# Kernel tuning notes

Hardware: AMD Instinct MI355X
Metric: run time of the kernel (lower is better)

## Reference

```python
import jax, jax.numpy as jnp
import numpy as np

N = 524288          # number of residues
N_RESTYPE = 21      # 20 amino acids + UNK
MAX_RIGID = 8       # rigid groups per residue (backbone + 7 torsion frames)
MAX_ATOM = 24       # max atoms per residue


def setup_inputs() -> dict:
    key = jax.random.key(0)
    ks = jax.random.split(key, 6)
    residue_type = jax.random.randint(ks[0], (N,), 0, N_RESTYPE)
    bb = jax.random.normal(ks[1], (N, 4, 3), jnp.float32)
    pos0 = jax.random.normal(ks[2], (N, 3), jnp.float32)
    sc = jax.random.normal(ks[3], (N, MAX_RIGID - 1, 2), jnp.float32)
    # learned/constant per-residue-type tables (RIGID_* in the original)
    transforms_tensor = jax.random.normal(ks[4], (N_RESTYPE, MAX_RIGID, 4, 3), jnp.float32) * 0.5
    rigids_tensor = jax.random.normal(ks[5], (N_RESTYPE, MAX_ATOM, 3), jnp.float32)
    rng = np.random.default_rng(0)
    td = np.zeros((N_RESTYPE, MAX_RIGID), dtype=np.int32)
    for i in range(1, MAX_RIGID):  # parent frame index must precede the group
        td[:, i] = rng.integers(0, i, size=N_RESTYPE)
    transforms_dep = jnp.asarray(td)
    rigids_dep = jnp.asarray(rng.integers(0, MAX_RIGID, size=(N_RESTYPE, MAX_ATOM)),
                             dtype=jnp.int32)
    return {
        "residue_type": residue_type, "bb": bb, "pos0": pos0, "sc": sc,
        "transforms_tensor": transforms_tensor, "rigids_tensor": rigids_tensor,
        "transforms_dep": transforms_dep, "rigids_dep": rigids_dep,
    }


def combine_operations(X, Y):
    # X, Y: [..., 4, 3] rigid operators (rows 0:3 rotation, row 3 translation)
    R = X[..., :3, :] @ Y[..., :3, :]
    t = jnp.einsum('...ij,...j->...i', X[..., :3, :], Y[..., 3, :]) + X[..., 3, :]
    return jnp.concatenate([R, t[..., None, :]], axis=-2)


def reference(residue_type, bb, pos0, sc,
              transforms_tensor, rigids_tensor, transforms_dep, rigids_dep):
    transforms = transforms_tensor[residue_type]   # [N, MAX_RIGID, 4, 3]
    t_dep = transforms_dep[residue_type]           # [N, MAX_RIGID]
    rigids = rigids_tensor[residue_type]           # [N, MAX_ATOM, 3]
    r_dep = rigids_dep[residue_type]               # [N, MAX_ATOM]
    n = bb.shape[0]

    # group 0: backbone frame; translation offset by pos0
    opr0 = jnp.concatenate([bb[:, :3], (bb[:, 3] + pos0)[:, None, :]], axis=1)  # [N,4,3]
    # groups 1..: x-axis rotation from (cos, sin) torsion pairs, zero translation
    c, s = sc[..., 0], sc[..., 1]
    z = jnp.zeros_like(c)
    o = jnp.ones_like(c)
    rot_x = jnp.stack([
        jnp.stack([o, z, z], -1),
        jnp.stack([z, c, -s], -1),
        jnp.stack([z, s, c], -1),
        jnp.stack([z, z, z], -1),
    ], axis=-2)                                    # [N, MAX_RIGID-1, 4, 3]
    opr = jnp.concatenate([opr0[:, None], rot_x], axis=1)  # [N, MAX_RIGID, 4, 3]

    # compose with per-group fixed transforms
    opr = combine_operations(transforms, opr)

    # sequential dependency-chain gather-compose over rigid groups (small fixed loop)
    idx = jnp.arange(n)
    for i_tor in range(1, MAX_RIGID):
        prev = opr[idx, t_dep[:, i_tor]]                 # [N, 4, 3]
        opr = opr.at[:, i_tor].set(combine_operations(prev, opr[:, i_tor]))

    # per-atom frame gather and coordinate placement
    opr_atom = opr[idx[:, None], r_dep]                  # [N, MAX_ATOM, 4, 3]
    R = jnp.einsum('naij,naj->nai', opr_atom[:, :, :3], rigids) + opr_atom[:, :, 3]
    return R, opr[:, 0]
```

## Files before the change

### kernel.cpp

```cpp
#include <hip/hip_runtime.h>

#define NRT 21
#define NRIG 8
#define NATOM 24
#define BLK 256

struct Op { float r[3][3]; float t[3]; };

__device__ __forceinline__ void combine(const Op& X, const Op& Y, Op& D) {
#pragma unroll
    for (int i = 0; i < 3; ++i) {
#pragma unroll
        for (int j = 0; j < 3; ++j)
            D.r[i][j] = X.r[i][0]*Y.r[0][j] + X.r[i][1]*Y.r[1][j] + X.r[i][2]*Y.r[2][j];
        D.t[i] = X.r[i][0]*Y.t[0] + X.r[i][1]*Y.t[1] + X.r[i][2]*Y.t[2] + X.t[i];
    }
}

__device__ __forceinline__ void mixop(const Op& a, const Op& b, bool c, Op& o) {
#pragma unroll
    for (int i = 0; i < 3; ++i) {
#pragma unroll
        for (int j = 0; j < 3; ++j) o.r[i][j] = c ? b.r[i][j] : a.r[i][j];
        o.t[i] = c ? b.t[i] : a.t[i];
    }
}

__device__ __forceinline__ void select8(const Op opr[NRIG], int d, Op& out) {
    out = opr[0];
#pragma unroll
    for (int k = 1; k < NRIG; ++k) mixop(out, opr[k], d == k, out);
}

__global__ __launch_bounds__(BLK) void backbone_kernel(
    const int*   __restrict__ rtyp,
    const float* __restrict__ bb,
    const float* __restrict__ pos0,
    const float* __restrict__ sc,
    const float* __restrict__ tf_g,
    const float* __restrict__ rg_g,
    const int*   __restrict__ td_g,
    const int*   __restrict__ rd_g,
    float* __restrict__ out,
    int N)
{
    __shared__ float s_tf[96 * NRT];
    __shared__ float s_rg[72 * NRT];
    __shared__ int   s_td[NRIG * NRT];
    __shared__ int   s_rd[NATOM * NRT];

    for (int i = threadIdx.x; i < 96 * NRT; i += BLK) {
        int rt = i / 96, k = i - rt * 96;
        s_tf[k * NRT + rt] = tf_g[i];
    }
    for (int i = threadIdx.x; i < 72 * NRT; i += BLK) {
        int rt = i / 72, k = i - rt * 72;
        s_rg[k * NRT + rt] = rg_g[i];
    }
    for (int i = threadIdx.x; i < NRIG * NRT; i += BLK) {
        int rt = i / NRIG, k = i - rt * NRIG;
        s_td[k * NRT + rt] = td_g[i];
    }
    for (int i = threadIdx.x; i < NATOM * NRT; i += BLK) {
        int rt = i / NATOM, k = i - rt * NATOM;
        s_rd[k * NRT + rt] = rd_g[i];
    }
    __syncthreads();

    int n = blockIdx.x * BLK + threadIdx.x;
    if (n >= N) return;
    int rt = rtyp[n];

    const float4* bb4 = (const float4*)(bb + (size_t)n * 12);
    float4 b0 = bb4[0], b1 = bb4[1], b2 = bb4[2];
    const float* pp = pos0 + (size_t)n * 3;
    float p0 = pp[0], p1 = pp[1], p2 = pp[2];

    const float2* sc2 = (const float2*)(sc + (size_t)n * 14);
    float2 cs[7];
#pragma unroll
    for (int i = 0; i < 7; ++i) cs[i] = sc2[i];

    Op opr[NRIG];

    {
        Op X;
#pragma unroll
        for (int r = 0; r < 3; ++r)
#pragma unroll
            for (int c = 0; c < 3; ++c)
                X.r[r][c] = s_tf[(r * 3 + c) * NRT + rt];
#pragma unroll
        for (int c = 0; c < 3; ++c) X.t[c] = s_tf[(9 + c) * NRT + rt];
        Op Y;
        Y.r[0][0] = b0.x; Y.r[0][1] = b0.y; Y.r[0][2] = b0.z;
        Y.r[1][0] = b0.w; Y.r[1][1] = b1.x; Y.r[1][2] = b1.y;
        Y.r[2][0] = b1.z; Y.r[2][1] = b1.w; Y.r[2][2] = b2.x;
        Y.t[0] = b2.y + p0; Y.t[1] = b2.z + p1; Y.t[2] = b2.w + p2;
        combine(X, Y, opr[0]);
    }

#pragma unroll
    for (int i = 1; i < NRIG; ++i) {
        Op X;
#pragma unroll
        for (int r = 0; r < 3; ++r)
#pragma unroll
            for (int c = 0; c < 3; ++c)
                X.r[r][c] = s_tf[(i * 12 + r * 3 + c) * NRT + rt];
#pragma unroll
        for (int c = 0; c < 3; ++c) X.t[c] = s_tf[(i * 12 + 9 + c) * NRT + rt];
        float cv = cs[i - 1].x;
        float sv = cs[i - 1].y;
#pragma unroll
        for (int r = 0; r < 3; ++r) {
            opr[i].r[r][0] = X.r[r][0];
            opr[i].r[r][1] = X.r[r][1] * cv + X.r[r][2] * sv;
            opr[i].r[r][2] = X.r[r][2] * cv - X.r[r][1] * sv;
            opr[i].t[r]    = X.t[r];
        }
    }

#pragma unroll
    for (int i = 1; i < NRIG; ++i) {
        int d = s_td[i * NRT + rt];
        Op prev = opr[0];
#pragma unroll
        for (int k = 1; k < NRIG; ++k) {
            if (k < i) mixop(prev, opr[k], d == k, prev);
        }
        Op res;
        combine(prev, opr[i], res);
        opr[i] = res;
    }

    float* outR = out + (size_t)n * 72;
#pragma unroll
    for (int ch = 0; ch < 6; ++ch) {
        float w[12];
#pragma unroll
        for (int q = 0; q < 4; ++q) {
            int a = ch * 4 + q;
            int d = s_rd[a * NRT + rt];
            Op T;
            select8(opr, d, T);
            float vx = s_rg[(a * 3 + 0) * NRT + rt];
            float vy = s_rg[(a * 3 + 1) * NRT + rt];
            float vz = s_rg[(a * 3 + 2) * NRT + rt];
            w[q * 3 + 0] = T.r[0][0] * vx + T.r[0][1] * vy + T.r[0][2] * vz + T.t[0];
            w[q * 3 + 1] = T.r[1][0] * vx + T.r[1][1] * vy + T.r[1][2] * vz + T.t[1];
            w[q * 3 + 2] = T.r[2][0] * vx + T.r[2][1] * vy + T.r[2][2] * vz + T.t[2];
        }
        float4* dst = (float4*)(outR + ch * 12);
        dst[0] = make_float4(w[0], w[1], w[2],  w[3]);
        dst[1] = make_float4(w[4], w[5], w[6],  w[7]);
        dst[2] = make_float4(w[8], w[9], w[10], w[11]);
    }

    {
        float4* df = (float4*)(out + (size_t)N * 72 + (size_t)n * 12);
        df[0] = make_float4(opr[0].r[0][0], opr[0].r[0][1], opr[0].r[0][2], opr[0].r[1][0]);
        df[1] = make_float4(opr[0].r[1][1], opr[0].r[1][2], opr[0].r[2][0], opr[0].r[2][1]);
        df[2] = make_float4(opr[0].r[2][2], opr[0].t[0],    opr[0].t[1],    opr[0].t[2]);
    }
}

extern "C" void kernel_launch(void* const* d_in, const int* in_sizes, int n_in,
                              void* d_out, int out_size, void* d_ws, size_t ws_size,
                              hipStream_t stream) {
    const int*   rtyp = (const int*)d_in[0];
    const float* bb   = (const float*)d_in[1];
    const float* pos0 = (const float*)d_in[2];
    const float* sc   = (const float*)d_in[3];
    const float* tf   = (const float*)d_in[4];
    const float* rg   = (const float*)d_in[5];
    const int*   td   = (const int*)d_in[6];
    const int*   rd   = (const int*)d_in[7];
    int N = in_sizes[0];
    int grid = (N + BLK - 1) / BLK;
    backbone_kernel<<<grid, BLK, 0, stream>>>(rtyp, bb, pos0, sc, tf, rg, td, rd,
                                              (float*)d_out, N);
}
```

Measured before the change: 300.6 us.

## Gather per-atom frames from fp16-packed shared memory instead of register selects

After the dependency chain, each thread writes its eight composed frames into shared memory, packed as half2 pairs. Each atom then loads the frame it needs by index, replacing the 8-way register select chain that ran for every atom. The dependency tables shrink to u8, and the launch bounds now ask for two blocks. The per-thread shared buffer is large, which caps occupancy. Rounding frames and translations to fp16 loses precision and may break the output tolerance.

```diff
diff --git a/kernel.cpp b/kernel.cpp
--- a/kernel.cpp
+++ b/kernel.cpp
@@ -1,10 +1,14 @@
 #include <hip/hip_runtime.h>
+#include <hip/hip_fp16.h>
 
 #define NRT 21
 #define NRIG 8
 #define NATOM 24
 #define BLK 256
 
+typedef unsigned int u32;
+typedef unsigned char u8;
+
 struct Op { float r[3][3]; float t[3]; };
 
 __device__ __forceinline__ void combine(const Op& X, const Op& Y, Op& D) {
@@ -26,13 +30,18 @@
     }
 }
 
-__device__ __forceinline__ void select8(const Op opr[NRIG], int d, Op& out) {
-    out = opr[0];
-#pragma unroll
-    for (int k = 1; k < NRIG; ++k) mixop(out, opr[k], d == k, out);
-}
-
-__global__ __launch_bounds__(BLK) void backbone_kernel(
+__device__ __forceinline__ u32 pk(float a, float b) {
+    __half2 h = __floats2half2_rn(a, b);
+    return __builtin_bit_cast(u32, h);
+}
+__device__ __forceinline__ float unlo(u32 w) {
+    __half2 h = __builtin_bit_cast(__half2, w); return __low2float(h);
+}
+__device__ __forceinline__ float unhi(u32 w) {
+    __half2 h = __builtin_bit_cast(__half2, w); return __high2float(h);
+}
+
+__global__ __launch_bounds__(BLK, 2) void backbone_kernel(
     const int*   __restrict__ rtyp,
     const float* __restrict__ bb,
     const float* __restrict__ pos0,
@@ -44,10 +53,11 @@
     float* __restrict__ out,
     int N)
 {
+    __shared__ u32   s_opr[48 * BLK];
     __shared__ float s_tf[96 * NRT];
     __shared__ float s_rg[72 * NRT];
-    __shared__ int   s_td[NRIG * NRT];
-    __shared__ int   s_rd[NATOM * NRT];
+    __shared__ u8    s_td[NRIG * NRT];
+    __shared__ u8    s_rd[NATOM * NRT];
 
     for (int i = threadIdx.x; i < 96 * NRT; i += BLK) {
         int rt = i / 96, k = i - rt * 96;
@@ -59,16 +69,17 @@
     }
     for (int i = threadIdx.x; i < NRIG * NRT; i += BLK) {
         int rt = i / NRIG, k = i - rt * NRIG;
-        s_td[k * NRT + rt] = td_g[i];
+        s_td[k * NRT + rt] = (u8)td_g[i];
     }
     for (int i = threadIdx.x; i < NATOM * NRT; i += BLK) {
         int rt = i / NATOM, k = i - rt * NATOM;
-        s_rd[k * NRT + rt] = rd_g[i];
+        s_rd[k * NRT + rt] = (u8)rd_g[i];
     }
     __syncthreads();
 
     int n = blockIdx.x * BLK + threadIdx.x;
     if (n >= N) return;
+    int t = threadIdx.x;
     int rt = rtyp[n];
 
     const float4* bb4 = (const float4*)(bb + (size_t)n * 12);
@@ -110,8 +121,7 @@
                 X.r[r][c] = s_tf[(i * 12 + r * 3 + c) * NRT + rt];
 #pragma unroll
         for (int c = 0; c < 3; ++c) X.t[c] = s_tf[(i * 12 + 9 + c) * NRT + rt];
-        float cv = cs[i - 1].x;
-        float sv = cs[i - 1].y;
+        float cv = cs[i - 1].x, sv = cs[i - 1].y;
 #pragma unroll
         for (int r = 0; r < 3; ++r) {
             opr[i].r[r][0] = X.r[r][0];
@@ -123,7 +133,7 @@
 
 #pragma unroll
     for (int i = 1; i < NRIG; ++i) {
-        int d = s_td[i * NRT + rt];
+        int d = (int)s_td[i * NRT + rt];
         Op prev = opr[0];
 #pragma unroll
         for (int k = 1; k < NRIG; ++k) {
@@ -134,6 +144,18 @@
         opr[i] = res;
     }
 
+#pragma unroll
+    for (int i = 0; i < NRIG; ++i) {
+        const Op& o = opr[i];
+        u32* dst = s_opr + (i * 6) * BLK + t;
+        dst[0 * BLK] = pk(o.r[0][0], o.r[0][1]);
+        dst[1 * BLK] = pk(o.r[0][2], o.r[1][0]);
+        dst[2 * BLK] = pk(o.r[1][1], o.r[1][2]);
+        dst[3 * BLK] = pk(o.r[2][0], o.r[2][1]);
+        dst[4 * BLK] = pk(o.r[2][2], o.t[0]);
+        dst[5 * BLK] = pk(o.t[1],    o.t[2]);
+    }
+
     float* outR = out + (size_t)n * 72;
 #pragma unroll
     for (int ch = 0; ch < 6; ++ch) {
@@ -141,15 +163,20 @@
 #pragma unroll
         for (int q = 0; q < 4; ++q) {
             int a = ch * 4 + q;
-            int d = s_rd[a * NRT + rt];
-            Op T;
-            select8(opr, d, T);
+            int d = (int)s_rd[a * NRT + rt];
+            const u32* src = s_opr + (d * 6) * BLK + t;
+            u32 w0 = src[0 * BLK], w1 = src[1 * BLK], w2 = src[2 * BLK];
+            u32 w3 = src[3 * BLK], w4 = src[4 * BLK], w5 = src[5 * BLK];
+            float r00 = unlo(w0), r01 = unhi(w0), r02 = unlo(w1);
+            float r10 = unhi(w1), r11 = unlo(w2), r12 = unhi(w2);
+            float r20 = unlo(w3), r21 = unhi(w3), r22 = unlo(w4);
+            float t0  = unhi(w4), t1  = unlo(w5), t2  = unhi(w5);
             float vx = s_rg[(a * 3 + 0) * NRT + rt];
             float vy = s_rg[(a * 3 + 1) * NRT + rt];
             float vz = s_rg[(a * 3 + 2) * NRT + rt];
-            w[q * 3 + 0] = T.r[0][0] * vx + T.r[0][1] * vy + T.r[0][2] * vz + T.t[0];
-            w[q * 3 + 1] = T.r[1][0] * vx + T.r[1][1] * vy + T.r[1][2] * vz + T.t[1];
-            w[q * 3 + 2] = T.r[2][0] * vx + T.r[2][1] * vy + T.r[2][2] * vz + T.t[2];
+            w[q * 3 + 0] = fmaf(r00, vx, fmaf(r01, vy, fmaf(r02, vz, t0)));
+            w[q * 3 + 1] = fmaf(r10, vx, fmaf(r11, vy, fmaf(r12, vz, t1)));
+            w[q * 3 + 2] = fmaf(r20, vx, fmaf(r21, vy, fmaf(r22, vz, t2)));
         }
         float4* dst = (float4*)(outR + ch * 12);
         dst[0] = make_float4(w[0], w[1], w[2],  w[3]);
```

After: 288.1 us. 4.2% less time.
